# Kernel tuning notes

Hardware: AMD Instinct MI355X
Metric: run time of the kernel (lower is better)

The kernel has to match this reference:

```python
import jax, jax.numpy as jnp
import numpy as np

B, Q, C, H = 4, 256, 1024, 128
NEG_SLOPE = 0.01  # F.leaky_relu default


def setup_inputs() -> dict:
    key = jax.random.key(0)
    ks = jax.random.split(key, 6)
    return {
        "query": jax.random.normal(ks[0], (B, Q, H), dtype=jnp.float32),
        "context": jax.random.normal(ks[1], (B, C, H), dtype=jnp.float32),
        "Ww": jax.random.normal(ks[2], (H, 2 * H), dtype=jnp.float32) * 0.05,
        "bw": jax.random.normal(ks[3], (H,), dtype=jnp.float32) * 0.05,
        "Ws": jax.random.normal(ks[4], (1, H), dtype=jnp.float32) * 0.05,
        "bs": jax.random.normal(ks[5], (1,), dtype=jnp.float32) * 0.05,
    }


def reference(query, context, Ww, bw, Ws, bs):
    # Faithful to: leaky_relu(Linear(cat(q_expand, c_expand))) then score, softmax, bmm.
    # cat+linear is split into per-input projections (mathematically identical),
    # avoiding the (B,Q,C,2H) concat materialization.
    h = query.shape[-1]
    Wq, Wc = Ww[:, :h], Ww[:, h:]
    hq = jnp.einsum('bqh,kh->bqk', query, Wq)            # (B,Q,H)
    hc = jnp.einsum('bch,kh->bck', context, Wc) + bw     # (B,C,H)
    hidden = jax.nn.leaky_relu(hq[:, :, None, :] + hc[:, None, :, :], NEG_SLOPE)  # (B,Q,C,H)
    score = jnp.einsum('bqch,oh->bqc', hidden, Ws) + bs[0]  # (B,Q,C)
    attn = jax.nn.softmax(score, axis=-1)                   # (B,Q,C)
    attn_output = jnp.einsum('bqc,bch->bqh', attn, context)  # mix=True bmm
    return (attn_output, attn)
```

## Files before the change

### kernel.cpp

```cpp
#include <hip/hip_runtime.h>

#define B_   4
#define Q_   256
#define C_   1024
#define H_   128

__global__ __launch_bounds__(128) void proj_kernel(
    const float* __restrict__ query, const float* __restrict__ context,
    const float* __restrict__ Ww, const float* __restrict__ bw,
    const float* __restrict__ Ws,
    float* __restrict__ hq, float* __restrict__ hc, float* __restrict__ dcv)
{
    __shared__ float dpar[2][4];

    const int blk = blockIdx.x;
    const int k = threadIdx.x;
    const bool is_q = (blk < (B_ * Q_ / 4));
    const int row0 = is_q ? (blk * 4) : ((blk - B_ * Q_ / 4) * 4);
    const float* __restrict__ in = is_q ? query : context;
    float* __restrict__ out = is_q ? hq : hc;

    const float4* __restrict__ Wrow =
        reinterpret_cast<const float4*>(Ww + k * (2 * H_) + (is_q ? 0 : H_));
    const float4* __restrict__ in4 =
        reinterpret_cast<const float4*>(in + row0 * H_);

    float acc[4] = {0.f, 0.f, 0.f, 0.f};
    #pragma unroll 4
    for (int h4 = 0; h4 < H_ / 4; ++h4) {
        const float4 w = Wrow[h4];
        #pragma unroll
        for (int r = 0; r < 4; ++r) {
            const float4 iv = in4[r * (H_ / 4) + h4];
            acc[r] += iv.x * w.x + iv.y * w.y + iv.z * w.z + iv.w * w.w;
        }
    }
    const float bias = is_q ? 0.f : bw[k];
    #pragma unroll
    for (int r = 0; r < 4; ++r) {
        acc[r] += bias;
        out[(row0 + r) * H_ + k] = acc[r];
    }

    if (!is_q) {
        const float wsk = Ws[k];
        float p[4];
        #pragma unroll
        for (int r = 0; r < 4; ++r) p[r] = wsk * acc[r];
        #pragma unroll
        for (int off = 32; off >= 1; off >>= 1) {
            #pragma unroll
            for (int r = 0; r < 4; ++r) p[r] += __shfl_xor(p[r], off, 64);
        }
        if ((k & 63) == 0) {
            #pragma unroll
            for (int r = 0; r < 4; ++r) dpar[k >> 6][r] = p[r];
        }
        __syncthreads();
        if (k < 4) dcv[row0 + k] = dpar[0][k] + dpar[1][k];
    }
}

__global__ __launch_bounds__(512) void attn_kernel(
    const float* __restrict__ hq, const float* __restrict__ hc,
    const float* __restrict__ Ws, const float* __restrict__ dcv,
    const float* __restrict__ context,
    float* __restrict__ outA, float* __restrict__ outP)
{
    const int b  = blockIdx.x & 3;
    const int q0 = (blockIdx.x >> 2) * 4;
    const int t  = threadIdx.x;
    const int wv = t >> 6;

    __shared__ float4 attn4_s[C_];
    __shared__ float  red[16 * 4 * H_];
    __shared__ float  s_hq[4][H_];
    __shared__ float  s_ws[H_];
    __shared__ float  wred[8][4];
    __shared__ float  wsum[8][4];

    const float4* __restrict__ ctx4 = reinterpret_cast<const float4*>(context);
    const int hg   = t & 31;
    const int crep = t >> 5;
    const int cb   = crep * 64;
    float4 pf[8];
    #pragma unroll
    for (int i = 0; i < 8; ++i)
        pf[i] = ctx4[(b * C_ + cb + i) * (H_ / 4) + hg];

    {
        const int q = t >> 7, k = t & 127;
        s_hq[q][k] = hq[(b * Q_ + q0 + q) * H_ + k];
        if (t < H_) s_ws[t] = Ws[t];
    }
    const int c0 = t, c1 = t + 512;
    const float dc0 = dcv[b * C_ + c0];
    const float dc1 = dcv[b * C_ + c1];
    __syncthreads();

    const float4* __restrict__ ws4 = reinterpret_cast<const float4*>(s_ws);
    const float4* __restrict__ hcp0 =
        reinterpret_cast<const float4*>(hc + (b * C_ + c0) * H_);
    const float4* __restrict__ hcp1 =
        reinterpret_cast<const float4*>(hc + (b * C_ + c1) * H_);

    float sabs[4][2] = {{0.f,0.f},{0.f,0.f},{0.f,0.f},{0.f,0.f}};
    #pragma unroll 4
    for (int k0 = 0; k0 < H_ / 4; ++k0) {
        const float4 wsv = ws4[k0];
        float4 hqv[4];
        #pragma unroll
        for (int q = 0; q < 4; ++q)
            hqv[q] = reinterpret_cast<const float4*>(s_hq[q])[k0];
        const float4 h0 = hcp0[k0];
        const float4 h1 = hcp1[k0];
        #pragma unroll
        for (int q = 0; q < 4; ++q) {
            sabs[q][0] += wsv.x * fabsf(hqv[q].x + h0.x)
                        + wsv.y * fabsf(hqv[q].y + h0.y)
                        + wsv.z * fabsf(hqv[q].z + h0.z)
                        + wsv.w * fabsf(hqv[q].w + h0.w);
            sabs[q][1] += wsv.x * fabsf(hqv[q].x + h1.x)
                        + wsv.y * fabsf(hqv[q].y + h1.y)
                        + wsv.z * fabsf(hqv[q].z + h1.z)
                        + wsv.w * fabsf(hqv[q].w + h1.w);
        }
    }
    float s[4][2];
    #pragma unroll
    for (int q = 0; q < 4; ++q) {
        s[q][0] = 0.505f * dc0 + 0.495f * sabs[q][0];
        s[q][1] = 0.505f * dc1 + 0.495f * sabs[q][1];
    }

    float m[4];
    #pragma unroll
    for (int q = 0; q < 4; ++q) {
        float v = fmaxf(s[q][0], s[q][1]);
        #pragma unroll
        for (int off = 32; off >= 1; off >>= 1)
            v = fmaxf(v, __shfl_xor(v, off, 64));
        m[q] = v;
    }
    if ((t & 63) == 0) {
        #pragma unroll
        for (int q = 0; q < 4; ++q) wred[wv][q] = m[q];
    }
    __syncthreads();
    #pragma unroll
    for (int q = 0; q < 4; ++q) {
        float v = wred[0][q];
        #pragma unroll
        for (int i = 1; i < 8; ++i) v = fmaxf(v, wred[i][q]);
        m[q] = v;
    }
    float e[4][2], p[4];
    #pragma unroll
    for (int q = 0; q < 4; ++q) {
        e[q][0] = __expf(s[q][0] - m[q]);
        e[q][1] = __expf(s[q][1] - m[q]);
        float v = e[q][0] + e[q][1];
        #pragma unroll
        for (int off = 32; off >= 1; off >>= 1)
            v += __shfl_xor(v, off, 64);
        p[q] = v;
    }
    if ((t & 63) == 0) {
        #pragma unroll
        for (int q = 0; q < 4; ++q) wsum[wv][q] = p[q];
    }
    __syncthreads();
    float rS[4];
    #pragma unroll
    for (int q = 0; q < 4; ++q) {
        float S = wsum[0][q];
        #pragma unroll
        for (int i = 1; i < 8; ++i) S += wsum[i][q];
        rS[q] = 1.0f / S;
    }
    float a0[4], a1[4];
    #pragma unroll
    for (int q = 0; q < 4; ++q) {
        a0[q] = e[q][0] * rS[q];
        a1[q] = e[q][1] * rS[q];
    }
    attn4_s[c0] = make_float4(a0[0], a0[1], a0[2], a0[3]);
    attn4_s[c1] = make_float4(a1[0], a1[1], a1[2], a1[3]);
    #pragma unroll
    for (int q = 0; q < 4; ++q) {
        outP[(b * Q_ + q0 + q) * C_ + c0] = a0[q];
        outP[(b * Q_ + q0 + q) * C_ + c1] = a1[q];
    }
    __syncthreads();

    float4 acc[4] = {{0,0,0,0},{0,0,0,0},{0,0,0,0},{0,0,0,0}};
    #pragma unroll
    for (int cc = 0; cc < 8; ++cc) {
        const float4 a4 = attn4_s[cb + cc];
        const float4 xv = pf[cc];
        acc[0].x += a4.x * xv.x; acc[0].y += a4.x * xv.y; acc[0].z += a4.x * xv.z; acc[0].w += a4.x * xv.w;
        acc[1].x += a4.y * xv.x; acc[1].y += a4.y * xv.y; acc[1].z += a4.y * xv.z; acc[1].w += a4.y * xv.w;
        acc[2].x += a4.z * xv.x; acc[2].y += a4.z * xv.y; acc[2].z += a4.z * xv.z; acc[2].w += a4.z * xv.w;
        acc[3].x += a4.w * xv.x; acc[3].y += a4.w * xv.y; acc[3].z += a4.w * xv.z; acc[3].w += a4.w * xv.w;
    }
    #pragma unroll 4
    for (int cc = 8; cc < 64; ++cc) {
        const int c = cb + cc;
        const float4 a4 = attn4_s[c];
        const float4 xv = ctx4[(b * C_ + c) * (H_ / 4) + hg];
        acc[0].x += a4.x * xv.x; acc[0].y += a4.x * xv.y; acc[0].z += a4.x * xv.z; acc[0].w += a4.x * xv.w;
        acc[1].x += a4.y * xv.x; acc[1].y += a4.y * xv.y; acc[1].z += a4.y * xv.z; acc[1].w += a4.y * xv.w;
        acc[2].x += a4.z * xv.x; acc[2].y += a4.z * xv.y; acc[2].z += a4.z * xv.z; acc[2].w += a4.z * xv.w;
        acc[3].x += a4.w * xv.x; acc[3].y += a4.w * xv.y; acc[3].z += a4.w * xv.z; acc[3].w += a4.w * xv.w;
    }
    float4* red4 = reinterpret_cast<float4*>(red);
    #pragma unroll
    for (int q = 0; q < 4; ++q)
        red4[(crep * 4 + q) * 32 + hg] = acc[q];
    __syncthreads();
    {
        const int q = t >> 7, h = t & 127;
        float v = 0.f;
        #pragma unroll
        for (int cr = 0; cr < 16; ++cr)
            v += red[(cr * 4 + q) * H_ + h];
        outA[(b * Q_ + q0 + q) * H_ + h] = v;
    }
}

extern "C" void kernel_launch(void* const* d_in, const int* in_sizes, int n_in,
                              void* d_out, int out_size, void* d_ws, size_t ws_size,
                              hipStream_t stream) {
    const float* query   = (const float*)d_in[0];
    const float* context = (const float*)d_in[1];
    const float* Ww      = (const float*)d_in[2];
    const float* bw      = (const float*)d_in[3];
    const float* Ws      = (const float*)d_in[4];

    float* outA = (float*)d_out;
    float* outP = outA + B_ * Q_ * H_;

    float* hq  = (float*)d_ws;
    float* hc  = hq + B_ * Q_ * H_;
    float* dcv = hc + B_ * C_ * H_;

    hipLaunchKernelGGL(proj_kernel, dim3(1280), dim3(128), 0, stream,
                       query, context, Ww, bw, Ws, hq, hc, dcv);
    hipLaunchKernelGGL(attn_kernel, dim3(256), dim3(512), 0, stream,
                       hq, hc, Ws, dcv, context, outA, outP);
}
```

Baseline: 102.8 us.

## Store context projection transposed for coalesced score loads and fold scale constants

```diff
diff --git a/kernel.cpp b/kernel.cpp
--- a/kernel.cpp
+++ b/kernel.cpp
@@ -5,20 +5,21 @@
 #define C_   1024
 #define H_   128
 
-__global__ __launch_bounds__(128) void proj_kernel(
+__global__ __launch_bounds__(256) void proj_kernel(
     const float* __restrict__ query, const float* __restrict__ context,
     const float* __restrict__ Ww, const float* __restrict__ bw,
     const float* __restrict__ Ws,
-    float* __restrict__ hq, float* __restrict__ hc, float* __restrict__ dcv)
+    float* __restrict__ hq, float* __restrict__ hcT, float* __restrict__ dcv)
 {
-    __shared__ float dpar[2][4];
-
-    const int blk = blockIdx.x;
-    const int k = threadIdx.x;
-    const bool is_q = (blk < (B_ * Q_ / 4));
-    const int row0 = is_q ? (blk * 4) : ((blk - B_ * Q_ / 4) * 4);
+    __shared__ float dpar[2][2][4];
+
+    const int blk  = blockIdx.x;
+    const int t    = threadIdx.x;
+    const int k    = t & 127;
+    const int half = t >> 7;
+    const bool is_q = (blk < (B_ * Q_ / 8));
+    const int row0 = (is_q ? blk * 8 : (blk - B_ * Q_ / 8) * 8) + half * 4;
     const float* __restrict__ in = is_q ? query : context;
-    float* __restrict__ out = is_q ? hq : hc;
 
     const float4* __restrict__ Wrow =
         reinterpret_cast<const float4*>(Ww + k * (2 * H_) + (is_q ? 0 : H_));
@@ -35,14 +36,21 @@
             acc[r] += iv.x * w.x + iv.y * w.y + iv.z * w.z + iv.w * w.w;
         }
     }
-    const float bias = is_q ? 0.f : bw[k];
-    #pragma unroll
-    for (int r = 0; r < 4; ++r) {
-        acc[r] += bias;
-        out[(row0 + r) * H_ + k] = acc[r];
-    }
-
-    if (!is_q) {
+
+    if (is_q) {
+        #pragma unroll
+        for (int r = 0; r < 4; ++r)
+            hq[(row0 + r) * H_ + k] = acc[r];
+    } else {
+        const float bias = bw[k];
+        #pragma unroll
+        for (int r = 0; r < 4; ++r) acc[r] += bias;
+
+        const int b  = row0 >> 10;
+        const int cl = row0 & (C_ - 1);
+        *reinterpret_cast<float4*>(hcT + (b * H_ + k) * C_ + cl) =
+            make_float4(acc[0], acc[1], acc[2], acc[3]);
+
         const float wsk = Ws[k];
         float p[4];
         #pragma unroll
@@ -54,15 +62,20 @@
         }
         if ((k & 63) == 0) {
             #pragma unroll
-            for (int r = 0; r < 4; ++r) dpar[k >> 6][r] = p[r];
+            for (int r = 0; r < 4; ++r) dpar[half][k >> 6][r] = p[r];
         }
         __syncthreads();
-        if (k < 4) dcv[row0 + k] = dpar[0][k] + dpar[1][k];
+        if (t < 8) {
+            const int hh = t >> 2, r = t & 3;
+            const int crow = (blk - B_ * Q_ / 8) * 8 + hh * 4 + r;
+            dcv[(crow >> 10) * C_ + (crow & (C_ - 1))] =
+                0.505f * (dpar[hh][0][r] + dpar[hh][1][r]);
+        }
     }
 }
 
 __global__ __launch_bounds__(512) void attn_kernel(
-    const float* __restrict__ hq, const float* __restrict__ hc,
+    const float* __restrict__ hq, const float* __restrict__ hcT,
     const float* __restrict__ Ws, const float* __restrict__ dcv,
     const float* __restrict__ context,
     float* __restrict__ outA, float* __restrict__ outP)
@@ -74,8 +87,8 @@
 
     __shared__ float4 attn4_s[C_];
     __shared__ float  red[16 * 4 * H_];
-    __shared__ float  s_hq[4][H_];
-    __shared__ float  s_ws[H_];
+    __shared__ __align__(16) float s_hq[4][H_];
+    __shared__ __align__(16) float s_ws[H_];
     __shared__ float  wred[8][4];
     __shared__ float  wsum[8][4];
 
@@ -89,48 +102,45 @@
         pf[i] = ctx4[(b * C_ + cb + i) * (H_ / 4) + hg];
 
     {
-        const int q = t >> 7, k = t & 127;
-        s_hq[q][k] = hq[(b * Q_ + q0 + q) * H_ + k];
-        if (t < H_) s_ws[t] = Ws[t];
-    }
-    const int c0 = t, c1 = t + 512;
+        const int q = t >> 7, kk = t & 127;
+        s_hq[q][kk] = hq[(b * Q_ + q0 + q) * H_ + kk];
+        if (t < H_) s_ws[t] = 0.495f * Ws[t];
+    }
+    const int c0 = 2 * t;
     const float dc0 = dcv[b * C_ + c0];
-    const float dc1 = dcv[b * C_ + c1];
+    const float dc1 = dcv[b * C_ + c0 + 1];
     __syncthreads();
 
     const float4* __restrict__ ws4 = reinterpret_cast<const float4*>(s_ws);
-    const float4* __restrict__ hcp0 =
-        reinterpret_cast<const float4*>(hc + (b * C_ + c0) * H_);
-    const float4* __restrict__ hcp1 =
-        reinterpret_cast<const float4*>(hc + (b * C_ + c1) * H_);
+    const float2* __restrict__ hcT2 =
+        reinterpret_cast<const float2*>(hcT + b * H_ * C_);
 
     float sabs[4][2] = {{0.f,0.f},{0.f,0.f},{0.f,0.f},{0.f,0.f}};
     #pragma unroll 4
-    for (int k0 = 0; k0 < H_ / 4; ++k0) {
-        const float4 wsv = ws4[k0];
-        float4 hqv[4];
-        #pragma unroll
-        for (int q = 0; q < 4; ++q)
-            hqv[q] = reinterpret_cast<const float4*>(s_hq[q])[k0];
-        const float4 h0 = hcp0[k0];
-        const float4 h1 = hcp1[k0];
+    for (int k4 = 0; k4 < H_ / 4; ++k4) {
+        const float4 wsv = ws4[k4];
+        float wk[4]  = {wsv.x, wsv.y, wsv.z, wsv.w};
+        float hqk[4][4];
         #pragma unroll
         for (int q = 0; q < 4; ++q) {
-            sabs[q][0] += wsv.x * fabsf(hqv[q].x + h0.x)
-                        + wsv.y * fabsf(hqv[q].y + h0.y)
-                        + wsv.z * fabsf(hqv[q].z + h0.z)
-                        + wsv.w * fabsf(hqv[q].w + h0.w);
-            sabs[q][1] += wsv.x * fabsf(hqv[q].x + h1.x)
-                        + wsv.y * fabsf(hqv[q].y + h1.y)
-                        + wsv.z * fabsf(hqv[q].z + h1.z)
-                        + wsv.w * fabsf(hqv[q].w + h1.w);
+            const float4 hv = reinterpret_cast<const float4*>(s_hq[q])[k4];
+            hqk[q][0] = hv.x; hqk[q][1] = hv.y; hqk[q][2] = hv.z; hqk[q][3] = hv.w;
+        }
+        #pragma unroll
+        for (int kk = 0; kk < 4; ++kk) {
+            const float2 hv = hcT2[(k4 * 4 + kk) * (C_ / 2) + t];
+            #pragma unroll
+            for (int q = 0; q < 4; ++q) {
+                sabs[q][0] += wk[kk] * fabsf(hqk[q][kk] + hv.x);
+                sabs[q][1] += wk[kk] * fabsf(hqk[q][kk] + hv.y);
+            }
         }
     }
     float s[4][2];
     #pragma unroll
     for (int q = 0; q < 4; ++q) {
-        s[q][0] = 0.505f * dc0 + 0.495f * sabs[q][0];
-        s[q][1] = 0.505f * dc1 + 0.495f * sabs[q][1];
+        s[q][0] = dc0 + sabs[q][0];
+        s[q][1] = dc1 + sabs[q][1];
     }
 
     float m[4];
@@ -184,12 +194,12 @@
         a0[q] = e[q][0] * rS[q];
         a1[q] = e[q][1] * rS[q];
     }
-    attn4_s[c0] = make_float4(a0[0], a0[1], a0[2], a0[3]);
-    attn4_s[c1] = make_float4(a1[0], a1[1], a1[2], a1[3]);
-    #pragma unroll
-    for (int q = 0; q < 4; ++q) {
-        outP[(b * Q_ + q0 + q) * C_ + c0] = a0[q];
-        outP[(b * Q_ + q0 + q) * C_ + c1] = a1[q];
+    attn4_s[c0]     = make_float4(a0[0], a0[1], a0[2], a0[3]);
+    attn4_s[c0 + 1] = make_float4(a1[0], a1[1], a1[2], a1[3]);
+    #pragma unroll
+    for (int q = 0; q < 4; ++q) {
+        *reinterpret_cast<float2*>(outP + (b * Q_ + q0 + q) * C_ + c0) =
+            make_float2(a0[q], a1[q]);
     }
     __syncthreads();
 
@@ -241,11 +251,11 @@
     float* outP = outA + B_ * Q_ * H_;
 
     float* hq  = (float*)d_ws;
-    float* hc  = hq + B_ * Q_ * H_;
-    float* dcv = hc + B_ * C_ * H_;
-
-    hipLaunchKernelGGL(proj_kernel, dim3(1280), dim3(128), 0, stream,
-                       query, context, Ww, bw, Ws, hq, hc, dcv);
+    float* hcT = hq + B_ * Q_ * H_;
+    float* dcv = hcT + B_ * H_ * C_;
+
+    hipLaunchKernelGGL(proj_kernel, dim3(640), dim3(256), 0, stream,
+                       query, context, Ww, bw, Ws, hq, hcT, dcv);
     hipLaunchKernelGGL(attn_kernel, dim3(256), dim3(512), 0, stream,
-                       hq, hc, Ws, dcv, context, outA, outP);
+                       hq, hcT, Ws, dcv, context, outA, outP);
 }
```

After: 121.5 us. +18.2%, slower.

## Use 1024-thread attention blocks with one context column per thread

Applied to the files above, without the earlier changes.

```diff
diff --git a/kernel.cpp b/kernel.cpp
--- a/kernel.cpp
+++ b/kernel.cpp
@@ -61,7 +61,7 @@
     }
 }
 
-__global__ __launch_bounds__(512) void attn_kernel(
+__global__ __launch_bounds__(1024) void attn_kernel(
     const float* __restrict__ hq, const float* __restrict__ hc,
     const float* __restrict__ Ws, const float* __restrict__ dcv,
     const float* __restrict__ context,
@@ -74,137 +74,94 @@
 
     __shared__ float4 attn4_s[C_];
     __shared__ float  red[16 * 4 * H_];
-    __shared__ float  s_hq[4][H_];
-    __shared__ float  s_ws[H_];
-    __shared__ float  wred[8][4];
-    __shared__ float  wsum[8][4];
+    __shared__ __align__(16) float s_hq[4][H_];
+    __shared__ __align__(16) float s_ws[H_];
+    __shared__ float  wred[16][4];
+    __shared__ float  wsum[16][4];
+
+    if (t < 512) {
+        const int q = t >> 7, kk = t & 127;
+        s_hq[q][kk] = hq[(b * Q_ + q0 + q) * H_ + kk];
+    }
+    if (t < H_) s_ws[t] = 0.495f * Ws[t];
+    const float dc = dcv[b * C_ + t];
+    __syncthreads();
+
+    const float4* __restrict__ ws4 = reinterpret_cast<const float4*>(s_ws);
+    const float4* __restrict__ hcp =
+        reinterpret_cast<const float4*>(hc + (b * C_ + t) * H_);
+
+    float sabs[4] = {0.f, 0.f, 0.f, 0.f};
+    #pragma unroll 4
+    for (int k4 = 0; k4 < H_ / 4; ++k4) {
+        const float4 wsv = ws4[k4];
+        const float4 hv  = hcp[k4];
+        #pragma unroll
+        for (int q = 0; q < 4; ++q) {
+            const float4 hqv = reinterpret_cast<const float4*>(s_hq[q])[k4];
+            sabs[q] += wsv.x * fabsf(hqv.x + hv.x)
+                     + wsv.y * fabsf(hqv.y + hv.y)
+                     + wsv.z * fabsf(hqv.z + hv.z)
+                     + wsv.w * fabsf(hqv.w + hv.w);
+        }
+    }
+    float s[4];
+    #pragma unroll
+    for (int q = 0; q < 4; ++q) s[q] = fmaf(0.505f, dc, sabs[q]);
+
+    float m[4];
+    #pragma unroll
+    for (int q = 0; q < 4; ++q) {
+        float v = s[q];
+        #pragma unroll
+        for (int off = 32; off >= 1; off >>= 1)
+            v = fmaxf(v, __shfl_xor(v, off, 64));
+        m[q] = v;
+    }
+    if ((t & 63) == 0) {
+        #pragma unroll
+        for (int q = 0; q < 4; ++q) wred[wv][q] = m[q];
+    }
+    __syncthreads();
+    #pragma unroll
+    for (int q = 0; q < 4; ++q) {
+        float v = wred[0][q];
+        #pragma unroll
+        for (int i = 1; i < 16; ++i) v = fmaxf(v, wred[i][q]);
+        m[q] = v;
+    }
+    float e[4];
+    #pragma unroll
+    for (int q = 0; q < 4; ++q) {
+        e[q] = __expf(s[q] - m[q]);
+        float v = e[q];
+        #pragma unroll
+        for (int off = 32; off >= 1; off >>= 1)
+            v += __shfl_xor(v, off, 64);
+        if ((t & 63) == 0) wsum[wv][q] = v;
+    }
+    __syncthreads();
+    float a[4];
+    #pragma unroll
+    for (int q = 0; q < 4; ++q) {
+        float S = wsum[0][q];
+        #pragma unroll
+        for (int i = 1; i < 16; ++i) S += wsum[i][q];
+        a[q] = e[q] * (1.0f / S);
+    }
+    attn4_s[t] = make_float4(a[0], a[1], a[2], a[3]);
+    #pragma unroll
+    for (int q = 0; q < 4; ++q)
+        outP[(b * Q_ + q0 + q) * C_ + t] = a[q];
+    __syncthreads();
 
     const float4* __restrict__ ctx4 = reinterpret_cast<const float4*>(context);
     const int hg   = t & 31;
     const int crep = t >> 5;
-    const int cb   = crep * 64;
-    float4 pf[8];
-    #pragma unroll
-    for (int i = 0; i < 8; ++i)
-        pf[i] = ctx4[(b * C_ + cb + i) * (H_ / 4) + hg];
-
-    {
-        const int q = t >> 7, k = t & 127;
-        s_hq[q][k] = hq[(b * Q_ + q0 + q) * H_ + k];
-        if (t < H_) s_ws[t] = Ws[t];
-    }
-    const int c0 = t, c1 = t + 512;
-    const float dc0 = dcv[b * C_ + c0];
-    const float dc1 = dcv[b * C_ + c1];
-    __syncthreads();
-
-    const float4* __restrict__ ws4 = reinterpret_cast<const float4*>(s_ws);
-    const float4* __restrict__ hcp0 =
-        reinterpret_cast<const float4*>(hc + (b * C_ + c0) * H_);
-    const float4* __restrict__ hcp1 =
-        reinterpret_cast<const float4*>(hc + (b * C_ + c1) * H_);
-
-    float sabs[4][2] = {{0.f,0.f},{0.f,0.f},{0.f,0.f},{0.f,0.f}};
+    const int cb   = crep * 32;
+    float4 acc[4] = {{0,0,0,0},{0,0,0,0},{0,0,0,0},{0,0,0,0}};
     #pragma unroll 4
-    for (int k0 = 0; k0 < H_ / 4; ++k0) {
-        const float4 wsv = ws4[k0];
-        float4 hqv[4];
-        #pragma unroll
-        for (int q = 0; q < 4; ++q)
-            hqv[q] = reinterpret_cast<const float4*>(s_hq[q])[k0];
-        const float4 h0 = hcp0[k0];
-        const float4 h1 = hcp1[k0];
-        #pragma unroll
-        for (int q = 0; q < 4; ++q) {
-            sabs[q][0] += wsv.x * fabsf(hqv[q].x + h0.x)
-                        + wsv.y * fabsf(hqv[q].y + h0.y)
-                        + wsv.z * fabsf(hqv[q].z + h0.z)
-                        + wsv.w * fabsf(hqv[q].w + h0.w);
-            sabs[q][1] += wsv.x * fabsf(hqv[q].x + h1.x)
-                        + wsv.y * fabsf(hqv[q].y + h1.y)
-                        + wsv.z * fabsf(hqv[q].z + h1.z)
-                        + wsv.w * fabsf(hqv[q].w + h1.w);
-        }
-    }
-    float s[4][2];
-    #pragma unroll
-    for (int q = 0; q < 4; ++q) {
-        s[q][0] = 0.505f * dc0 + 0.495f * sabs[q][0];
-        s[q][1] = 0.505f * dc1 + 0.495f * sabs[q][1];
-    }
-
-    float m[4];
-    #pragma unroll
-    for (int q = 0; q < 4; ++q) {
-        float v = fmaxf(s[q][0], s[q][1]);
-        #pragma unroll
-        for (int off = 32; off >= 1; off >>= 1)
-            v = fmaxf(v, __shfl_xor(v, off, 64));
-        m[q] = v;
-    }
-    if ((t & 63) == 0) {
-        #pragma unroll
-        for (int q = 0; q < 4; ++q) wred[wv][q] = m[q];
-    }
-    __syncthreads();
-    #pragma unroll
-    for (int q = 0; q < 4; ++q) {
-        float v = wred[0][q];
-        #pragma unroll
-        for (int i = 1; i < 8; ++i) v = fmaxf(v, wred[i][q]);
-        m[q] = v;
-    }
-    float e[4][2], p[4];
-    #pragma unroll
-    for (int q = 0; q < 4; ++q) {
-        e[q][0] = __expf(s[q][0] - m[q]);
-        e[q][1] = __expf(s[q][1] - m[q]);
-        float v = e[q][0] + e[q][1];
-        #pragma unroll
-        for (int off = 32; off >= 1; off >>= 1)
-            v += __shfl_xor(v, off, 64);
-        p[q] = v;
-    }
-    if ((t & 63) == 0) {
-        #pragma unroll
-        for (int q = 0; q < 4; ++q) wsum[wv][q] = p[q];
-    }
-    __syncthreads();
-    float rS[4];
-    #pragma unroll
-    for (int q = 0; q < 4; ++q) {
-        float S = wsum[0][q];
-        #pragma unroll
-        for (int i = 1; i < 8; ++i) S += wsum[i][q];
-        rS[q] = 1.0f / S;
-    }
-    float a0[4], a1[4];
-    #pragma unroll
-    for (int q = 0; q < 4; ++q) {
-        a0[q] = e[q][0] * rS[q];
-        a1[q] = e[q][1] * rS[q];
-    }
-    attn4_s[c0] = make_float4(a0[0], a0[1], a0[2], a0[3]);
-    attn4_s[c1] = make_float4(a1[0], a1[1], a1[2], a1[3]);
-    #pragma unroll
-    for (int q = 0; q < 4; ++q) {
-        outP[(b * Q_ + q0 + q) * C_ + c0] = a0[q];
-        outP[(b * Q_ + q0 + q) * C_ + c1] = a1[q];
-    }
-    __syncthreads();
-
-    float4 acc[4] = {{0,0,0,0},{0,0,0,0},{0,0,0,0},{0,0,0,0}};
-    #pragma unroll
-    for (int cc = 0; cc < 8; ++cc) {
-        const float4 a4 = attn4_s[cb + cc];
-        const float4 xv = pf[cc];
-        acc[0].x += a4.x * xv.x; acc[0].y += a4.x * xv.y; acc[0].z += a4.x * xv.z; acc[0].w += a4.x * xv.w;
-        acc[1].x += a4.y * xv.x; acc[1].y += a4.y * xv.y; acc[1].z += a4.y * xv.z; acc[1].w += a4.y * xv.w;
-        acc[2].x += a4.z * xv.x; acc[2].y += a4.z * xv.y; acc[2].z += a4.z * xv.z; acc[2].w += a4.z * xv.w;
-        acc[3].x += a4.w * xv.x; acc[3].y += a4.w * xv.y; acc[3].z += a4.w * xv.z; acc[3].w += a4.w * xv.w;
-    }
-    #pragma unroll 4
-    for (int cc = 8; cc < 64; ++cc) {
+    for (int cc = 0; cc < 32; ++cc) {
         const int c = cb + cc;
         const float4 a4 = attn4_s[c];
         const float4 xv = ctx4[(b * C_ + c) * (H_ / 4) + hg];
@@ -214,11 +171,23 @@
         acc[3].x += a4.w * xv.x; acc[3].y += a4.w * xv.y; acc[3].z += a4.w * xv.z; acc[3].w += a4.w * xv.w;
     }
     float4* red4 = reinterpret_cast<float4*>(red);
-    #pragma unroll
-    for (int q = 0; q < 4; ++q)
-        red4[(crep * 4 + q) * 32 + hg] = acc[q];
-    __syncthreads();
-    {
+    if (crep < 16) {
+        #pragma unroll
+        for (int q = 0; q < 4; ++q)
+            red4[(crep * 4 + q) * 32 + hg] = acc[q];
+    }
+    __syncthreads();
+    if (crep >= 16) {
+        #pragma unroll
+        for (int q = 0; q < 4; ++q) {
+            const int idx = ((crep - 16) * 4 + q) * 32 + hg;
+            float4 r = red4[idx];
+            r.x += acc[q].x; r.y += acc[q].y; r.z += acc[q].z; r.w += acc[q].w;
+            red4[idx] = r;
+        }
+    }
+    __syncthreads();
+    if (t < 512) {
         const int q = t >> 7, h = t & 127;
         float v = 0.f;
         #pragma unroll
@@ -246,6 +215,6 @@
 
     hipLaunchKernelGGL(proj_kernel, dim3(1280), dim3(128), 0, stream,
                        query, context, Ww, bw, Ws, hq, hc, dcv);
-    hipLaunchKernelGGL(attn_kernel, dim3(256), dim3(512), 0, stream,
+    hipLaunchKernelGGL(attn_kernel, dim3(256), dim3(1024), 0, stream,
                        hq, hc, Ws, dcv, context, outA, outP);
 }
```

Result: no change. 104.4 us (+1.6%).
